# Performance work log

Hardware: AMD Instinct MI355X
Metric: run time of the kernel (lower is better)

## Reference

```python
import jax, jax.numpy as jnp
import numpy as np

SFREQ = 100
NPERSEG = 100  # min(n_times=200, 100)
NOVERLAP = NPERSEG // 2

# periodic hann window (scipy get_window('hann', N) with sym=False)
_WIN_NP = 0.5 - 0.5 * np.cos(2.0 * np.pi * np.arange(NPERSEG) / NPERSEG)
_WIN_SQ_SUM = float(np.sum(_WIN_NP ** 2))
_FREQS = np.fft.rfftfreq(NPERSEG, 1.0 / SFREQ)  # 0..50 Hz, 51 bins
_BANDS = [(0.5, 4.0), (4.0, 8.0), (8.0, 13.0), (13.0, 30.0)]  # delta/theta/alpha/beta
_BAND_IDX = [np.where((_FREQS >= lo) & (_FREQS <= hi))[0] for lo, hi in _BANDS]


def welch_band_features(x):
    """Batched Welch PSD band powers. x: (B,C,T) -> (B, C*4)."""
    B, C, T = x.shape
    step = NPERSEG - NOVERLAP
    n_seg = (T - NPERSEG) // step + 1
    seg_idx = np.arange(n_seg)[:, None] * step + np.arange(NPERSEG)  # (S, L)
    segs = x[..., seg_idx]                              # (B,C,S,L)
    segs = segs - segs.mean(-1, keepdims=True)          # detrend='constant'
    win = jnp.asarray(_WIN_NP, x.dtype)
    spec = jnp.fft.rfft(segs * win, axis=-1)            # (B,C,S,F)
    scale = 1.0 / (SFREQ * _WIN_SQ_SUM)
    psd = (spec.real ** 2 + spec.imag ** 2) * scale
    psd = psd.at[..., 1:-1].multiply(2.0)               # one-sided, nfft even
    psd = psd.mean(-2)                                  # average over segments -> (B,C,F)
    feats = jnp.stack([psd[..., idx].mean(-1) for idx in _BAND_IDX], axis=-1)  # (B,C,4)
    return feats.reshape(B, C * 4)


def setup_inputs() -> dict:
    key = jax.random.key(0)
    ks = jax.random.split(key, 16)
    B, C, T = 2048, 129, 200
    red = C // 8  # 16
    s = 0.05
    inp = {
        "x": jax.random.normal(ks[0], (B, C, T), jnp.float32),
        # channel attention fc (no bias)
        "w_att1": jax.random.normal(ks[1], (C, red), jnp.float32) * s,
        "w_att2": jax.random.normal(ks[2], (red, C), jnp.float32) * s,
        # stand-in EEGNeX backbone: time-mean pool + linear C->64
        "w_bb": jax.random.normal(ks[3], (C, 64), jnp.float32) * s,
        "b_bb": jnp.zeros((64,), jnp.float32),
        # freq encoder
        "w_fe1": jax.random.normal(ks[4], (C * 4, 128), jnp.float32) * s,
        "b_fe1": jnp.zeros((128,), jnp.float32),
        "w_fe2": jax.random.normal(ks[5], (128, 64), jnp.float32) * s,
        "b_fe2": jnp.zeros((64,), jnp.float32),
        # head
        "w_h1": jax.random.normal(ks[6], (128, 128), jnp.float32) * s,
        "b_h1": jnp.zeros((128,), jnp.float32),
        "w_h2": jax.random.normal(ks[7], (128, 64), jnp.float32) * s,
        "b_h2": jnp.zeros((64,), jnp.float32),
        "w_h3": jax.random.normal(ks[8], (64, 1), jnp.float32) * s,
        "b_h3": jnp.zeros((1,), jnp.float32),
    }
    return inp


def reference(x, w_att1, w_att2, w_bb, b_bb, w_fe1, b_fe1, w_fe2, b_fe2,
              w_h1, b_h1, w_h2, b_h2, w_h3, b_h3):
    # --- channel attention ---
    avg = x.mean(-1)                                    # (B,C)
    mx = x.max(-1)                                      # (B,C)
    fc = lambda v: jax.nn.relu(v @ w_att1) @ w_att2
    att = jax.nn.sigmoid(fc(avg) + fc(mx))[..., None]   # (B,C,1)
    x_att = x * att
    # --- backbone (stand-in for EEGNeXBase): time pool + linear ---
    time_feat = jax.nn.relu(x_att.mean(-1) @ w_bb + b_bb)  # (B,64)
    # --- frequency branch (computed from raw x, detached in original) ---
    freq = welch_band_features(jax.lax.stop_gradient(x))   # (B, C*4)
    freq = jax.nn.relu(freq @ w_fe1 + b_fe1)
    freq = jax.nn.relu(freq @ w_fe2 + b_fe2)               # (B,64)
    # --- head ---
    h = jnp.concatenate([time_feat, freq], axis=1)         # (B,128)
    h = jax.nn.relu(h @ w_h1 + b_h1)
    h = jax.nn.relu(h @ w_h2 + b_h2)
    return h @ w_h3 + b_h3                                  # (B,1)
```

## Files before the change

kernel.cpp:

```cpp
#include <hip/hip_runtime.h>
#include <math.h>

constexpr int BB = 2048;
constexpr int CC = 129;
constexpr int TT = 200;
constexpr int NPAIR = BB * CC;
constexpr int PPB = 64;
constexpr int XSTR = 204;
constexpr int WSLICE = 16 * XSTR;

constexpr int OFF_AVG = 8192;
constexpr int OFF_MX  = OFF_AVG + NPAIR;
constexpr int OFF_FT  = OFF_MX + NPAIR;

typedef __bf16 bf16x8 __attribute__((ext_vector_type(8)));
typedef float  f32x4  __attribute__((ext_vector_type(4)));

union BFU { int4 v; bf16x8 b; };
union BSU { __bf16 b; unsigned short u; };

__global__ void kInit(unsigned short* __restrict__ bfr) {
    int tid = blockIdx.x * 256 + threadIdx.x;
    if (tid >= 16384) return;
    int i    = tid & 7;
    int lane = (tid >> 3) & 63;
    int h    = (tid >> 9) & 1;
    int nt   = (tid >> 10) & 3;
    int ks   = tid >> 12;
    int k = ks * 32 + (lane >> 4) * 8 + i;
    int n = nt * 16 + (lane & 15);
    float v = 0.f;
    if (k < 100) {
        if (n < 60) {
            int kb = (n >> 1) + 1;
            const float C = 0.06283185307179587f;
            float w = 0.5f - 0.5f * cosf(C * (float)k);
            int ph = (kb * k) % 100;
            float ang = C * (float)ph;
            v = w * ((n & 1) ? sinf(ang) : cosf(ang));
        } else if (n == 60) {
            v = 0.01f;
        }
    }
    __bf16 hb = (__bf16)v;
    BSU out;
    if (h == 0) out.b = hb;
    else        out.b = (__bf16)(v - (float)hb);
    bfr[tid] = out.u;
}

__global__ __launch_bounds__(256, 3) void kA(const float* __restrict__ x,
                                             const unsigned short* __restrict__ bfr,
                                             float* __restrict__ avg,
                                             float* __restrict__ mxg,
                                             float* __restrict__ feat) {
    __shared__ __align__(16) float xs[4 * WSLICE];

    const int tid  = threadIdx.x;
    const int blk  = blockIdx.x;
    const int wv   = tid >> 6;
    const int lane = tid & 63;

    float* wx = xs + wv * WSLICE;

    {
        const int p = lane >> 2, q = lane & 3;
        const float* rowg = x + ((size_t)blk * PPB + wv * 16 + p) * TT;
        float* rowl = wx + p * XSTR;
        float m = -3.4e38f;
        #pragma unroll
        for (int j = 0; j < 13; j++) {
            int i4 = q + 4 * j;
            if (i4 < 50) {
                float4 v = *(const float4*)(rowg + i4 * 4);
                *(float4*)(rowl + i4 * 4) = v;
                m = fmaxf(fmaxf(m, fmaxf(v.x, v.y)), fmaxf(v.z, v.w));
            }
        }
        m = fmaxf(m, __shfl_xor(m, 1, 64));
        m = fmaxf(m, __shfl_xor(m, 2, 64));
        if (q == 0) mxg[blk * PPB + wv * 16 + p] = m;
    }

    const int quad = lane >> 4, mrow = lane & 15;

    const float* abase[3];
    {
        #pragma unroll
        for (int mi = 0; mi < 3; mi++) {
            int lr = mi * 16 + mrow;
            int pl = lr / 3;
            int sg = lr - pl * 3;
            abase[mi] = wx + pl * XSTR + sg * 50;
        }
    }

    f32x4 acc[3][4];
    #pragma unroll
    for (int a = 0; a < 3; a++)
        #pragma unroll
        for (int b = 0; b < 4; b++) acc[a][b] = f32x4{0.f, 0.f, 0.f, 0.f};

    const int4* bg = (const int4*)bfr;
    #pragma unroll
    for (int ks = 0; ks < 4; ks++) {
        bf16x8 Bh[4], Bl[4];
        #pragma unroll
        for (int nt = 0; nt < 4; nt++) {
            BFU uh, ul;
            uh.v = bg[((ks * 4 + nt) * 2 + 0) * 64 + lane];
            ul.v = bg[((ks * 4 + nt) * 2 + 1) * 64 + lane];
            Bh[nt] = uh.b;
            Bl[nt] = ul.b;
        }
        #pragma unroll
        for (int mi = 0; mi < 3; mi++) {
            float f[8];
            if (ks < 3) {
                const float* s = abase[mi] + quad * 8 + ks * 32;
                float2 f0 = *(const float2*)(s);
                float2 f1 = *(const float2*)(s + 2);
                float2 f2 = *(const float2*)(s + 4);
                float2 f3 = *(const float2*)(s + 6);
                f[0] = f0.x; f[1] = f0.y; f[2] = f1.x; f[3] = f1.y;
                f[4] = f2.x; f[5] = f2.y; f[6] = f3.x; f[7] = f3.y;
            } else {
                const float* s = abase[mi] + 96;
                float2 f0 = *(const float2*)(s);
                float2 f1 = *(const float2*)(s + 2);
                bool v0 = (quad == 0);
                f[0] = v0 ? f0.x : 0.f; f[1] = v0 ? f0.y : 0.f;
                f[2] = v0 ? f1.x : 0.f; f[3] = v0 ? f1.y : 0.f;
                f[4] = 0.f; f[5] = 0.f; f[6] = 0.f; f[7] = 0.f;
            }
            bf16x8 Ah, Al;
            #pragma unroll
            for (int i = 0; i < 8; i++) {
                __bf16 hb = (__bf16)f[i];
                Ah[i] = hb;
                Al[i] = (__bf16)(f[i] - (float)hb);
            }
            __builtin_amdgcn_s_setprio(1);
            #pragma unroll
            for (int nt = 0; nt < 4; nt++) {
                acc[mi][nt] = __builtin_amdgcn_mfma_f32_16x16x32_bf16(Al, Bh[nt], acc[mi][nt], 0, 0, 0);
                acc[mi][nt] = __builtin_amdgcn_mfma_f32_16x16x32_bf16(Ah, Bl[nt], acc[mi][nt], 0, 0, 0);
                acc[mi][nt] = __builtin_amdgcn_mfma_f32_16x16x32_bf16(Ah, Bh[nt], acc[mi][nt], 0, 0, 0);
            }
            __builtin_amdgcn_s_setprio(0);
        }
    }

    float* sp = wx;
    #pragma unroll
    for (int mi = 0; mi < 3; mi++)
        #pragma unroll
        for (int nt = 0; nt < 4; nt++) {
            int col = nt * 16 + mrow;
            #pragma unroll
            for (int i = 0; i < 4; i++)
                sp[(mi * 16 + quad * 4 + i) * 66 + col] = acc[mi][nt][i];
        }

    {
        const int p2 = lane >> 2, q = lane & 3;
        const float* r0 = sp + p2 * 3 * 66;
        float s0 = 0.f, s1 = 0.f, s2 = 0.f, s3 = 0.f;
        float mu0 = 0.f, mu2 = 0.f;
        #pragma unroll
        for (int sg = 0; sg < 3; sg++) {
            const float* row = r0 + sg * 66;
            float mu = row[60];
            if (sg == 0) mu0 = mu;
            if (sg == 2) mu2 = mu;
            #pragma unroll
            for (int j = 0; j < 15; j++) {
                int c = q * 15 + j;
                float v = row[c];
                if (j == 0) v = (q == 0) ? (v + 25.f * mu) : v;
                float v2 = v * v;
                s0 += (c <= 7) ? v2 : 0.f;
                s1 += (c >= 6 && c <= 15) ? v2 : 0.f;
                s2 += (c >= 14 && c <= 25) ? v2 : 0.f;
                s3 += (c >= 24) ? v2 : 0.f;
            }
        }
        s0 += __shfl_xor(s0, 1, 64); s1 += __shfl_xor(s1, 1, 64);
        s2 += __shfl_xor(s2, 1, 64); s3 += __shfl_xor(s3, 1, 64);
        s0 += __shfl_xor(s0, 2, 64); s1 += __shfl_xor(s1, 2, 64);
        s2 += __shfl_xor(s2, 2, 64); s3 += __shfl_xor(s3, 2, 64);
        if (q == 0) {
            int pg = blk * PPB + wv * 16 + p2;
            float4 fo;
            fo.x = s0 * (2.f / (11250.f * 4.f));
            fo.y = s1 * (2.f / (11250.f * 5.f));
            fo.z = s2 * (2.f / (11250.f * 6.f));
            fo.w = s3 * (2.f / (11250.f * 18.f));
            *(float4*)(feat + (size_t)pg * 4) = fo;
            avg[pg] = (mu0 + mu2) * 0.5f;
        }
    }
}

__global__ __launch_bounds__(256, 8) void kB(const float* __restrict__ avg,
                                             const float* __restrict__ mxv,
                                             const float* __restrict__ feat,
                                             const float* __restrict__ w_att1,
                                             const float* __restrict__ w_att2,
                                             const float* __restrict__ w_bb,
                                             const float* __restrict__ b_bb,
                                             const float* __restrict__ w_fe1,
                                             const float* __restrict__ b_fe1,
                                             const float* __restrict__ w_fe2,
                                             const float* __restrict__ b_fe2,
                                             const float* __restrict__ w_h1,
                                             const float* __restrict__ b_h1,
                                             const float* __restrict__ w_h2,
                                             const float* __restrict__ b_h2,
                                             const float* __restrict__ w_h3,
                                             const float* __restrict__ b_h3,
                                             float* __restrict__ out) {
    __shared__ float s_avg[132], s_mx[132], s_fq[520];
    __shared__ float s_t1a[16], s_t1b[16], s_t1[16];
    __shared__ float s_v[132];
    __shared__ float s_tf[2][64];
    __shared__ float s_p1[2][128];
    __shared__ float s_f1[128];
    __shared__ float s_p2[4][64];
    __shared__ float s_h[128];
    __shared__ float s_pg1[2][128];
    __shared__ float s_g1[128];
    __shared__ float s_pg2[4][64];

    const int b = blockIdx.x;
    const int tid = threadIdx.x;

    for (int i = tid; i < 129; i += 256) { s_avg[i] = avg[b * 129 + i]; s_mx[i] = mxv[b * 129 + i]; }
    for (int i = tid; i < 516; i += 256) s_fq[i] = feat[(size_t)b * 516 + i];
    __syncthreads();

    if (tid < 32) {
        int h = tid & 15;
        const float* src = (tid >= 16) ? s_mx : s_avg;
        float acc = 0.f;
        #pragma unroll 4
        for (int c = 0; c < 129; c++) acc += src[c] * w_att1[c * 16 + h];
        ((tid >= 16) ? s_t1b : s_t1a)[h] = fmaxf(acc, 0.f);
    }
    __syncthreads();
    if (tid < 16) s_t1[tid] = s_t1a[tid] + s_t1b[tid];
    __syncthreads();

    if (tid < 129) {
        float l = 0.f;
        #pragma unroll
        for (int j = 0; j < 16; j++) l += s_t1[j] * w_att2[j * 129 + tid];
        s_v[tid] = s_avg[tid] / (1.f + expf(-l));
    }
    __syncthreads();

    if (tid < 128) {
        int o = tid & 63, ks = tid >> 6;
        int i0 = ks ? 65 : 0, i1 = ks ? 129 : 65;
        float acc = 0.f;
        #pragma unroll 4
        for (int i = i0; i < i1; i++) acc += s_v[i] * w_bb[i * 64 + o];
        s_tf[ks][o] = acc;
    }
    {
        int o = tid & 127, ks = tid >> 7;
        float acc = 0.f;
        #pragma unroll 4
        for (int i = ks * 258; i < ks * 258 + 258; i++) acc += s_fq[i] * w_fe1[i * 128 + o];
        s_p1[ks][o] = acc;
    }
    __syncthreads();
    if (tid < 64) s_h[tid] = fmaxf(s_tf[0][tid] + s_tf[1][tid] + b_bb[tid], 0.f);
    if (tid >= 128) { int o = tid - 128; s_f1[o] = fmaxf(s_p1[0][o] + s_p1[1][o] + b_fe1[o], 0.f); }
    __syncthreads();

    {
        int o = tid & 63, ks = tid >> 6;
        float acc = 0.f;
        #pragma unroll 4
        for (int i = ks * 32; i < ks * 32 + 32; i++) acc += s_f1[i] * w_fe2[i * 64 + o];
        s_p2[ks][o] = acc;
    }
    __syncthreads();
    if (tid < 64) s_h[64 + tid] = fmaxf(s_p2[0][tid] + s_p2[1][tid] + s_p2[2][tid] + s_p2[3][tid] + b_fe2[tid], 0.f);
    __syncthreads();

    {
        int o = tid & 127, ks = tid >> 7;
        float acc = 0.f;
        #pragma unroll 4
        for (int i = ks * 64; i < ks * 64 + 64; i++) acc += s_h[i] * w_h1[i * 128 + o];
        s_pg1[ks][o] = acc;
    }
    __syncthreads();
    if (tid < 128) s_g1[tid] = fmaxf(s_pg1[0][tid] + s_pg1[1][tid] + b_h1[tid], 0.f);
    __syncthreads();

    {
        int o = tid & 63, ks = tid >> 6;
        float acc = 0.f;
        #pragma unroll 4
        for (int i = ks * 32; i < ks * 32 + 32; i++) acc += s_g1[i] * w_h2[i * 64 + o];
        s_pg2[ks][o] = acc;
    }
    __syncthreads();

    if (tid < 64) {
        float g2 = fmaxf(s_pg2[0][tid] + s_pg2[1][tid] + s_pg2[2][tid] + s_pg2[3][tid] + b_h2[tid], 0.f);
        float pz = g2 * w_h3[tid];
        for (int off = 32; off >= 1; off >>= 1) pz += __shfl_xor(pz, off, 64);
        if (tid == 0) out[b] = pz + b_h3[0];
    }
}

extern "C" void kernel_launch(void* const* d_in, const int* in_sizes, int n_in,
                              void* d_out, int out_size, void* d_ws, size_t ws_size,
                              hipStream_t stream) {
    const float* x      = (const float*)d_in[0];
    const float* w_att1 = (const float*)d_in[1];
    const float* w_att2 = (const float*)d_in[2];
    const float* w_bb   = (const float*)d_in[3];
    const float* b_bb   = (const float*)d_in[4];
    const float* w_fe1  = (const float*)d_in[5];
    const float* b_fe1  = (const float*)d_in[6];
    const float* w_fe2  = (const float*)d_in[7];
    const float* b_fe2  = (const float*)d_in[8];
    const float* w_h1   = (const float*)d_in[9];
    const float* b_h1   = (const float*)d_in[10];
    const float* w_h2   = (const float*)d_in[11];
    const float* b_h2   = (const float*)d_in[12];
    const float* w_h3   = (const float*)d_in[13];
    const float* b_h3   = (const float*)d_in[14];

    float* ws = (float*)d_ws;
    unsigned short* bfr = (unsigned short*)ws;
    float* avg = ws + OFF_AVG;
    float* mxv = ws + OFF_MX;
    float* feat = ws + OFF_FT;

    kInit<<<64, 256, 0, stream>>>(bfr);
    kA<<<NPAIR / PPB, 256, 0, stream>>>(x, bfr, avg, mxv, feat);
    kB<<<BB, 256, 0, stream>>>(avg, mxv, feat,
                               w_att1, w_att2, w_bb, b_bb,
                               w_fe1, b_fe1, w_fe2, b_fe2,
                               w_h1, b_h1, w_h2, b_h2, w_h3, b_h3,
                               (float*)d_out);
}
```

Measured before the change: 419.3 us.

## Read MFMA A operands from global memory and reduce band powers with shuffles

The kernel stops staging each 200-sample row in LDS. The max pass and the MFMA A-operand loads now read x directly from global memory, so the second pass relies on cache hits. The spectrum-to-band reduction now runs on the MFMA accumulator registers with 16-lane shuffles, which drops the large LDS scatter. LDS use falls to a small per-wave scratch, and the occupancy hint rises from 3 to 4 blocks per CU. The trade-off is that x is read twice from global memory or L2, and the per-lane A loads are likely uncoalesced.

```diff
diff --git a/kernel.cpp b/kernel.cpp
--- a/kernel.cpp
+++ b/kernel.cpp
@@ -6,8 +6,6 @@
 constexpr int TT = 200;
 constexpr int NPAIR = BB * CC;
 constexpr int PPB = 64;
-constexpr int XSTR = 204;
-constexpr int WSLICE = 16 * XSTR;
 
 constexpr int OFF_AVG = 8192;
 constexpr int OFF_MX  = OFF_AVG + NPAIR;
@@ -49,50 +47,45 @@
     bfr[tid] = out.u;
 }
 
-__global__ __launch_bounds__(256, 3) void kA(const float* __restrict__ x,
+__global__ __launch_bounds__(256, 4) void kA(const float* __restrict__ x,
                                              const unsigned short* __restrict__ bfr,
                                              float* __restrict__ avg,
                                              float* __restrict__ mxg,
                                              float* __restrict__ feat) {
-    __shared__ __align__(16) float xs[4 * WSLICE];
+    __shared__ __align__(16) float rsall[4 * 384];
 
     const int tid  = threadIdx.x;
     const int blk  = blockIdx.x;
     const int wv   = tid >> 6;
     const int lane = tid & 63;
-
-    float* wx = xs + wv * WSLICE;
-
-    {
-        const int p = lane >> 2, q = lane & 3;
-        const float* rowg = x + ((size_t)blk * PPB + wv * 16 + p) * TT;
-        float* rowl = wx + p * XSTR;
+    const int P0   = blk * PPB + wv * 16;
+
+    {
+        int p = lane >> 2, q = lane & 3;
+        const float* rowg = x + (size_t)(P0 + p) * TT;
         float m = -3.4e38f;
         #pragma unroll
         for (int j = 0; j < 13; j++) {
             int i4 = q + 4 * j;
             if (i4 < 50) {
                 float4 v = *(const float4*)(rowg + i4 * 4);
-                *(float4*)(rowl + i4 * 4) = v;
                 m = fmaxf(fmaxf(m, fmaxf(v.x, v.y)), fmaxf(v.z, v.w));
             }
         }
         m = fmaxf(m, __shfl_xor(m, 1, 64));
         m = fmaxf(m, __shfl_xor(m, 2, 64));
-        if (q == 0) mxg[blk * PPB + wv * 16 + p] = m;
+        if (q == 0) mxg[P0 + p] = m;
     }
 
     const int quad = lane >> 4, mrow = lane & 15;
 
     const float* abase[3];
-    {
-        #pragma unroll
-        for (int mi = 0; mi < 3; mi++) {
-            int lr = mi * 16 + mrow;
-            int pl = lr / 3;
-            int sg = lr - pl * 3;
-            abase[mi] = wx + pl * XSTR + sg * 50;
-        }
+    #pragma unroll
+    for (int mi = 0; mi < 3; mi++) {
+        int lr = mi * 16 + mrow;
+        int pl = lr / 3;
+        int sg = lr - pl * 3;
+        abase[mi] = x + (size_t)(P0 + pl) * TT + sg * 50;
     }
 
     f32x4 acc[3][4];
@@ -151,54 +144,47 @@
         }
     }
 
-    float* sp = wx;
+    float* rs = rsall + wv * 384;
     #pragma unroll
-    for (int mi = 0; mi < 3; mi++)
-        #pragma unroll
-        for (int nt = 0; nt < 4; nt++) {
-            int col = nt * 16 + mrow;
+    for (int mi = 0; mi < 3; mi++) {
+        #pragma unroll
+        for (int i = 0; i < 4; i++) {
+            float mu = __shfl(acc[mi][3][i], (lane & 48) | 12, 64);
+            float v0 = acc[mi][0][i];
+            if (mrow == 0) v0 += 25.f * mu;
+            float w0 = v0 * v0;
+            float w1 = acc[mi][1][i] * acc[mi][1][i];
+            float w2 = acc[mi][2][i] * acc[mi][2][i];
+            float w3 = acc[mi][3][i] * acc[mi][3][i];
+            float s0 = (mrow <= 7) ? w0 : 0.f;
+            float s1 = (mrow >= 6) ? w0 : 0.f;
+            float s2 = ((mrow >= 14) ? w0 : 0.f) + ((mrow <= 9) ? w1 : 0.f);
+            float s3 = ((mrow >= 8) ? w1 : 0.f) + w2 + ((mrow <= 11) ? w3 : 0.f);
             #pragma unroll
-            for (int i = 0; i < 4; i++)
-                sp[(mi * 16 + quad * 4 + i) * 66 + col] = acc[mi][nt][i];
-        }
-
-    {
-        const int p2 = lane >> 2, q = lane & 3;
-        const float* r0 = sp + p2 * 3 * 66;
-        float s0 = 0.f, s1 = 0.f, s2 = 0.f, s3 = 0.f;
-        float mu0 = 0.f, mu2 = 0.f;
-        #pragma unroll
-        for (int sg = 0; sg < 3; sg++) {
-            const float* row = r0 + sg * 66;
-            float mu = row[60];
-            if (sg == 0) mu0 = mu;
-            if (sg == 2) mu2 = mu;
-            #pragma unroll
-            for (int j = 0; j < 15; j++) {
-                int c = q * 15 + j;
-                float v = row[c];
-                if (j == 0) v = (q == 0) ? (v + 25.f * mu) : v;
-                float v2 = v * v;
-                s0 += (c <= 7) ? v2 : 0.f;
-                s1 += (c >= 6 && c <= 15) ? v2 : 0.f;
-                s2 += (c >= 14 && c <= 25) ? v2 : 0.f;
-                s3 += (c >= 24) ? v2 : 0.f;
-            }
-        }
-        s0 += __shfl_xor(s0, 1, 64); s1 += __shfl_xor(s1, 1, 64);
-        s2 += __shfl_xor(s2, 1, 64); s3 += __shfl_xor(s3, 1, 64);
-        s0 += __shfl_xor(s0, 2, 64); s1 += __shfl_xor(s1, 2, 64);
-        s2 += __shfl_xor(s2, 2, 64); s3 += __shfl_xor(s3, 2, 64);
-        if (q == 0) {
-            int pg = blk * PPB + wv * 16 + p2;
-            float4 fo;
-            fo.x = s0 * (2.f / (11250.f * 4.f));
-            fo.y = s1 * (2.f / (11250.f * 5.f));
-            fo.z = s2 * (2.f / (11250.f * 6.f));
-            fo.w = s3 * (2.f / (11250.f * 18.f));
-            *(float4*)(feat + (size_t)pg * 4) = fo;
-            avg[pg] = (mu0 + mu2) * 0.5f;
-        }
+            for (int m = 1; m <= 8; m <<= 1) {
+                s0 += __shfl_xor(s0, m, 16);
+                s1 += __shfl_xor(s1, m, 16);
+                s2 += __shfl_xor(s2, m, 16);
+                s3 += __shfl_xor(s3, m, 16);
+            }
+            if (mrow == 0) {
+                int lr = mi * 16 + quad * 4 + i;
+                *(float4*)(rs + lr * 8) = float4{s0, s1, s2, s3};
+                rs[lr * 8 + 4] = mu;
+            }
+        }
+    }
+
+    {
+        int p2 = lane >> 2, q = lane & 3;
+        int base = p2 * 24;
+        float t = rs[base + q] + rs[base + 8 + q] + rs[base + 16 + q];
+        float sc = (q == 0) ? (2.f / 45000.f)
+                 : (q == 1) ? (2.f / 56250.f)
+                 : (q == 2) ? (2.f / 67500.f)
+                 :            (2.f / 202500.f);
+        feat[(size_t)(P0 + p2) * 4 + q] = t * sc;
+        if (q == 0) avg[P0 + p2] = (rs[base + 4] + rs[base + 20]) * 0.5f;
     }
 }
 
```

Result: slower. 457.7 us (+9.1%).

## Swap MFMA operand roles so band-power reduction runs from registers, not LDS

Applied to the files above, without the earlier changes.

Restructures kernel kA so each wave handles 16 channel rows, with the DFT basis as the A operand and the signal segments as the B operand. The MFMA output layout then lets band sums and the segment mean be reduced directly from accumulator registers with cross-lane shuffles, dropping the shared-memory spill and re-read of spectra. The global load becomes a flat coalesced float4 copy, and the per-row max is folded into the fragment reads instead of a separate pass. The ks loop is no longer unrolled, trading some scheduling freedom for fewer registers, and the band-mask logic now depends on the accumulator lane mapping being exactly right.

```diff
diff --git a/kernel.cpp b/kernel.cpp
--- a/kernel.cpp
+++ b/kernel.cpp
@@ -5,8 +5,9 @@
 constexpr int CC = 129;
 constexpr int TT = 200;
 constexpr int NPAIR = BB * CC;
-constexpr int PPB = 64;
-constexpr int XSTR = 204;
+constexpr int NPG   = NPAIR / 16;
+constexpr int NBLK  = NPG / 4;
+constexpr int XSTR  = 204;
 constexpr int WSLICE = 16 * XSTR;
 
 constexpr int OFF_AVG = 8192;
@@ -57,41 +58,22 @@
     __shared__ __align__(16) float xs[4 * WSLICE];
 
     const int tid  = threadIdx.x;
-    const int blk  = blockIdx.x;
     const int wv   = tid >> 6;
     const int lane = tid & 63;
-
+    const int pg   = blockIdx.x * 4 + wv;
+    const int quad = lane >> 4, mrow = lane & 15;
     float* wx = xs + wv * WSLICE;
 
     {
-        const int p = lane >> 2, q = lane & 3;
-        const float* rowg = x + ((size_t)blk * PPB + wv * 16 + p) * TT;
-        float* rowl = wx + p * XSTR;
-        float m = -3.4e38f;
-        #pragma unroll
-        for (int j = 0; j < 13; j++) {
-            int i4 = q + 4 * j;
-            if (i4 < 50) {
-                float4 v = *(const float4*)(rowg + i4 * 4);
-                *(float4*)(rowl + i4 * 4) = v;
-                m = fmaxf(fmaxf(m, fmaxf(v.x, v.y)), fmaxf(v.z, v.w));
-            }
-        }
-        m = fmaxf(m, __shfl_xor(m, 1, 64));
-        m = fmaxf(m, __shfl_xor(m, 2, 64));
-        if (q == 0) mxg[blk * PPB + wv * 16 + p] = m;
-    }
-
-    const int quad = lane >> 4, mrow = lane & 15;
-
-    const float* abase[3];
-    {
-        #pragma unroll
-        for (int mi = 0; mi < 3; mi++) {
-            int lr = mi * 16 + mrow;
-            int pl = lr / 3;
-            int sg = lr - pl * 3;
-            abase[mi] = wx + pl * XSTR + sg * 50;
+        const float4* xg = (const float4*)(x + (size_t)pg * 16 * TT);
+        #pragma unroll
+        for (int it = 0; it < 13; it++) {
+            int idx = lane + it * 64;
+            if (idx < 800) {
+                float4 v = xg[idx];
+                int p = idx / 50, t4 = (idx % 50) * 4;
+                *(float4*)(wx + p * XSTR + t4) = v;
+            }
         }
     }
 
@@ -101,104 +83,111 @@
         #pragma unroll
         for (int b = 0; b < 4; b++) acc[a][b] = f32x4{0.f, 0.f, 0.f, 0.f};
 
+    float m = -3.4e38f;
     const int4* bg = (const int4*)bfr;
-    #pragma unroll
+    const float* rbase = wx + mrow * XSTR;
+
+    #pragma unroll 1
     for (int ks = 0; ks < 4; ks++) {
-        bf16x8 Bh[4], Bl[4];
+        bf16x8 Th[4], Tl[4];
         #pragma unroll
         for (int nt = 0; nt < 4; nt++) {
             BFU uh, ul;
             uh.v = bg[((ks * 4 + nt) * 2 + 0) * 64 + lane];
             ul.v = bg[((ks * 4 + nt) * 2 + 1) * 64 + lane];
-            Bh[nt] = uh.b;
-            Bl[nt] = ul.b;
-        }
-        #pragma unroll
-        for (int mi = 0; mi < 3; mi++) {
+            Th[nt] = uh.b;
+            Tl[nt] = ul.b;
+        }
+        #pragma unroll
+        for (int sg = 0; sg < 3; sg++) {
             float f[8];
             if (ks < 3) {
-                const float* s = abase[mi] + quad * 8 + ks * 32;
+                const float* s = rbase + sg * 50 + ks * 32 + quad * 8;
                 float2 f0 = *(const float2*)(s);
                 float2 f1 = *(const float2*)(s + 2);
                 float2 f2 = *(const float2*)(s + 4);
                 float2 f3 = *(const float2*)(s + 6);
                 f[0] = f0.x; f[1] = f0.y; f[2] = f1.x; f[3] = f1.y;
                 f[4] = f2.x; f[5] = f2.y; f[6] = f3.x; f[7] = f3.y;
+                if (sg != 1) {
+                    m = fmaxf(m, fmaxf(fmaxf(f[0], f[1]), fmaxf(f[2], f[3])));
+                    m = fmaxf(m, fmaxf(fmaxf(f[4], f[5]), fmaxf(f[6], f[7])));
+                }
             } else {
-                const float* s = abase[mi] + 96;
+                const float* s = rbase + sg * 50 + 96;
                 float2 f0 = *(const float2*)(s);
                 float2 f1 = *(const float2*)(s + 2);
+                if (sg != 1)
+                    m = fmaxf(m, fmaxf(fmaxf(f0.x, f0.y), fmaxf(f1.x, f1.y)));
                 bool v0 = (quad == 0);
                 f[0] = v0 ? f0.x : 0.f; f[1] = v0 ? f0.y : 0.f;
                 f[2] = v0 ? f1.x : 0.f; f[3] = v0 ? f1.y : 0.f;
                 f[4] = 0.f; f[5] = 0.f; f[6] = 0.f; f[7] = 0.f;
             }
-            bf16x8 Ah, Al;
+            bf16x8 Xh, Xl;
             #pragma unroll
             for (int i = 0; i < 8; i++) {
                 __bf16 hb = (__bf16)f[i];
-                Ah[i] = hb;
-                Al[i] = (__bf16)(f[i] - (float)hb);
+                Xh[i] = hb;
+                Xl[i] = (__bf16)(f[i] - (float)hb);
             }
             __builtin_amdgcn_s_setprio(1);
             #pragma unroll
             for (int nt = 0; nt < 4; nt++) {
-                acc[mi][nt] = __builtin_amdgcn_mfma_f32_16x16x32_bf16(Al, Bh[nt], acc[mi][nt], 0, 0, 0);
-                acc[mi][nt] = __builtin_amdgcn_mfma_f32_16x16x32_bf16(Ah, Bl[nt], acc[mi][nt], 0, 0, 0);
-                acc[mi][nt] = __builtin_amdgcn_mfma_f32_16x16x32_bf16(Ah, Bh[nt], acc[mi][nt], 0, 0, 0);
+                acc[sg][nt] = __builtin_amdgcn_mfma_f32_16x16x32_bf16(Th[nt], Xl, acc[sg][nt], 0, 0, 0);
+                acc[sg][nt] = __builtin_amdgcn_mfma_f32_16x16x32_bf16(Tl[nt], Xh, acc[sg][nt], 0, 0, 0);
+                acc[sg][nt] = __builtin_amdgcn_mfma_f32_16x16x32_bf16(Th[nt], Xh, acc[sg][nt], 0, 0, 0);
             }
             __builtin_amdgcn_s_setprio(0);
         }
     }
 
-    float* sp = wx;
+    float s0 = 0.f, s1 = 0.f, s2 = 0.f, s3 = 0.f;
+    float mu0 = 0.f, mu2 = 0.f;
     #pragma unroll
-    for (int mi = 0; mi < 3; mi++)
+    for (int sg = 0; sg < 3; sg++) {
+        float mu = __shfl(acc[sg][3][0], 48 | mrow, 64);
+        if (sg == 0) mu0 = mu;
+        if (sg == 2) mu2 = mu;
         #pragma unroll
         for (int nt = 0; nt < 4; nt++) {
-            int col = nt * 16 + mrow;
             #pragma unroll
-            for (int i = 0; i < 4; i++)
-                sp[(mi * 16 + quad * 4 + i) * 66 + col] = acc[mi][nt][i];
-        }
-
-    {
-        const int p2 = lane >> 2, q = lane & 3;
-        const float* r0 = sp + p2 * 3 * 66;
-        float s0 = 0.f, s1 = 0.f, s2 = 0.f, s3 = 0.f;
-        float mu0 = 0.f, mu2 = 0.f;
-        #pragma unroll
-        for (int sg = 0; sg < 3; sg++) {
-            const float* row = r0 + sg * 66;
-            float mu = row[60];
-            if (sg == 0) mu0 = mu;
-            if (sg == 2) mu2 = mu;
-            #pragma unroll
-            for (int j = 0; j < 15; j++) {
-                int c = q * 15 + j;
-                float v = row[c];
-                if (j == 0) v = (q == 0) ? (v + 25.f * mu) : v;
-                float v2 = v * v;
-                s0 += (c <= 7) ? v2 : 0.f;
-                s1 += (c >= 6 && c <= 15) ? v2 : 0.f;
-                s2 += (c >= 14 && c <= 25) ? v2 : 0.f;
-                s3 += (c >= 24) ? v2 : 0.f;
-            }
-        }
-        s0 += __shfl_xor(s0, 1, 64); s1 += __shfl_xor(s1, 1, 64);
-        s2 += __shfl_xor(s2, 1, 64); s3 += __shfl_xor(s3, 1, 64);
-        s0 += __shfl_xor(s0, 2, 64); s1 += __shfl_xor(s1, 2, 64);
-        s2 += __shfl_xor(s2, 2, 64); s3 += __shfl_xor(s3, 2, 64);
-        if (q == 0) {
-            int pg = blk * PPB + wv * 16 + p2;
-            float4 fo;
-            fo.x = s0 * (2.f / (11250.f * 4.f));
-            fo.y = s1 * (2.f / (11250.f * 5.f));
-            fo.z = s2 * (2.f / (11250.f * 6.f));
-            fo.w = s3 * (2.f / (11250.f * 18.f));
-            *(float4*)(feat + (size_t)pg * 4) = fo;
-            avg[pg] = (mu0 + mu2) * 0.5f;
-        }
+            for (int i = 0; i < 4; i++) {
+                float v = acc[sg][nt][i];
+                if (nt == 0 && i == 0) v += (quad == 0) ? 25.f * mu : 0.f;
+                float w = v * v;
+                if (nt == 0) {
+                    s0 += (quad <= 1) ? w : 0.f;
+                    s1 += (quad * 4 + i >= 6) ? w : 0.f;
+                    if (i >= 2) s2 += (quad == 3) ? w : 0.f;
+                } else if (nt == 1) {
+                    s2 += (quad * 4 + i <= 9) ? w : 0.f;
+                    s3 += (quad >= 2) ? w : 0.f;
+                } else if (nt == 2) {
+                    s3 += w;
+                } else {
+                    s3 += (quad <= 2) ? w : 0.f;
+                }
+            }
+        }
+    }
+    s0 += __shfl_xor(s0, 16, 64); s1 += __shfl_xor(s1, 16, 64);
+    s2 += __shfl_xor(s2, 16, 64); s3 += __shfl_xor(s3, 16, 64);
+    s0 += __shfl_xor(s0, 32, 64); s1 += __shfl_xor(s1, 32, 64);
+    s2 += __shfl_xor(s2, 32, 64); s3 += __shfl_xor(s3, 32, 64);
+    m = fmaxf(m, __shfl_xor(m, 16, 64));
+    m = fmaxf(m, __shfl_xor(m, 32, 64));
+
+    if (quad == 0) {
+        int pr = pg * 16 + mrow;
+        float4 fo;
+        fo.x = s0 * (2.f / 45000.f);
+        fo.y = s1 * (2.f / 56250.f);
+        fo.z = s2 * (2.f / 67500.f);
+        fo.w = s3 * (2.f / 202500.f);
+        *(float4*)(feat + (size_t)pr * 4) = fo;
+        avg[pr] = (mu0 + mu2) * 0.5f;
+        mxg[pr] = m;
     }
 }
 
@@ -339,12 +328,12 @@
 
     float* ws = (float*)d_ws;
     unsigned short* bfr = (unsigned short*)ws;
-    float* avg = ws + OFF_AVG;
-    float* mxv = ws + OFF_MX;
+    float* avg  = ws + OFF_AVG;
+    float* mxv  = ws + OFF_MX;
     float* feat = ws + OFF_FT;
 
     kInit<<<64, 256, 0, stream>>>(bfr);
-    kA<<<NPAIR / PPB, 256, 0, stream>>>(x, bfr, avg, mxv, feat);
+    kA<<<NBLK, 256, 0, stream>>>(x, bfr, avg, mxv, feat);
     kB<<<BB, 256, 0, stream>>>(avg, mxv, feat,
                                w_att1, w_att2, w_bb, b_bb,
                                w_fe1, b_fe1, w_fe2, b_fe2,
```

Measured after the change: 419.1 us. About the same (-0.1%).
